# Kernel tuning notes

Measured on AMD Instinct MI355X. Metric: run time of the kernel, lower is better.

The kernel has to match this reference:

```python
import jax, jax.numpy as jnp
import numpy as np

D, H1, O, E = 1024, 4096, 1024, 8
B = 8192


def setup_inputs() -> dict:
    key = jax.random.key(0)
    k1, k2, k3, k4 = jax.random.split(key, 4)
    # kaiming_uniform_ with nonlinearity='relu': bound = sqrt(6 / fan_in), fan_in = last dim
    b_w1 = float(np.sqrt(6.0 / D))
    b_w2 = float(np.sqrt(6.0 / H1))
    x = jax.random.normal(k1, (B, D), dtype=jnp.float32)
    eid = jax.random.randint(k2, (B,), 0, E, dtype=jnp.int32)
    W1 = jax.random.uniform(k3, (E, H1, D), dtype=jnp.float32, minval=-b_w1, maxval=b_w1)
    W2 = jax.random.uniform(k4, (E, O, H1), dtype=jnp.float32, minval=-b_w2, maxval=b_w2)
    b2 = jnp.zeros((E, O), dtype=jnp.float32)
    return {"x": x, "eid": eid, "W1": W1, "W2": W2, "b2": b2}


def reference(x, eid, W1, W2, b2):
    # Per-token expert MLP: y_i = gelu(x_i @ W1[eid_i].T) @ W2[eid_i].T + b2[eid_i]
    # Dense-dispatch formulation: loop over the (small, static) expert axis,
    # compute each expert MLP on all tokens, and select per-token via mask.
    # Math is identical to the sort/gather/scatter original.
    y = jnp.zeros((x.shape[0], W2.shape[1]), dtype=x.dtype)
    for e in range(W1.shape[0]):
        h = jax.nn.gelu(x @ W1[e].T, approximate=False)   # [B, H1]
        y_e = h @ W2[e].T + b2[e]                          # [B, O]
        mask = (eid == e)[:, None].astype(x.dtype)
        y = y + mask * y_e
    return y
```

## Files before the change

kernel.cpp:

```cpp
#include <hip/hip_runtime.h>
#include <hip/hip_bf16.h>
#include <math.h>

constexpr int kD  = 1024;
constexpr int kH1 = 4096;
constexpr int kO  = 1024;
constexpr int kE  = 8;
constexpr int kB  = 8192;

constexpr int BM = 256;
constexpr int MAXT = kB / BM + kE;

typedef __attribute__((ext_vector_type(8))) short short8;
typedef __attribute__((ext_vector_type(4))) float f32x4;

__device__ __forceinline__ unsigned short f2bf(float f) {
  unsigned int u = __float_as_uint(f);
  u += 0x7fffu + ((u >> 16) & 1u);
  return (unsigned short)(u >> 16);
}

__device__ __forceinline__ float gelu_fast(float x) {
  float u = 0.7978845608028654f * (x + 0.044715f * x * x * x);
  float eu = __expf(2.0f * u);
  float th = 1.0f - 2.0f / (eu + 1.0f);
  return 0.5f * x * (1.0f + th);
}

__global__ __launch_bounds__(256) void setup_kernel(const int* __restrict__ eid,
                                                    int* __restrict__ perm,
                                                    int* __restrict__ tiles) {
  __shared__ int cnt[kE];
  __shared__ int off[kE];
  __shared__ int cur[kE];
  int t = threadIdx.x;
  if (t < kE) { cnt[t] = 0; cur[t] = 0; }
  __syncthreads();
  for (int i = t; i < kB; i += 256) atomicAdd(&cnt[eid[i]], 1);
  __syncthreads();
  if (t == 0) {
    int o = 0, nt = 0;
    for (int e = 0; e < kE; ++e) {
      off[e] = o;
      int c = cnt[e];
      for (int r = 0; r < c; r += BM) {
        tiles[nt * 4 + 0] = e;
        tiles[nt * 4 + 1] = o + r;
        tiles[nt * 4 + 2] = (c - r < BM) ? (c - r) : BM;
        tiles[nt * 4 + 3] = 0;
        ++nt;
      }
      o += c;
    }
    for (; nt < MAXT; ++nt) {
      tiles[nt * 4 + 0] = 0; tiles[nt * 4 + 1] = 0;
      tiles[nt * 4 + 2] = 0; tiles[nt * 4 + 3] = 0;
    }
  }
  __syncthreads();
  for (int i = t; i < kB; i += 256) {
    int e = eid[i];
    int p = off[e] + atomicAdd(&cur[e], 1);
    perm[p] = i;
  }
}

__global__ __launch_bounds__(256) void gather_kernel(const float* __restrict__ x,
                                                     const int* __restrict__ perm,
                                                     unsigned short* __restrict__ xg) {
  int idx = blockIdx.x * 256 + threadIdx.x;
  int pos = idx >> 7;
  int c   = (idx & 127) << 3;
  int row = perm[pos];
  const float4* s = (const float4*)(x + (size_t)row * kD + c);
  float4 f0 = s[0], f1 = s[1];
  short8 v;
  v[0] = (short)f2bf(f0.x); v[1] = (short)f2bf(f0.y);
  v[2] = (short)f2bf(f0.z); v[3] = (short)f2bf(f0.w);
  v[4] = (short)f2bf(f1.x); v[5] = (short)f2bf(f1.y);
  v[6] = (short)f2bf(f1.z); v[7] = (short)f2bf(f1.w);
  *(short8*)(xg + (size_t)pos * kD + c) = v;
}

__global__ __launch_bounds__(256) void convert_kernel(const float* __restrict__ src,
                                                      unsigned short* __restrict__ dst,
                                                      int n8) {
  int stride = gridDim.x * 256;
  for (int i = blockIdx.x * 256 + threadIdx.x; i < n8; i += stride) {
    const float4* s = (const float4*)(src + (size_t)i * 8);
    float4 f0 = s[0], f1 = s[1];
    short8 v;
    v[0] = (short)f2bf(f0.x); v[1] = (short)f2bf(f0.y);
    v[2] = (short)f2bf(f0.z); v[3] = (short)f2bf(f0.w);
    v[4] = (short)f2bf(f1.x); v[5] = (short)f2bf(f1.y);
    v[6] = (short)f2bf(f1.z); v[7] = (short)f2bf(f1.w);
    *(short8*)(dst + (size_t)i * 8) = v;
  }
}

template <int K, int N, bool GELU, bool BIAS, bool OUTBF>
__global__ __launch_bounds__(512, 2) void gemm8p_kernel(
    const unsigned short* __restrict__ Amat,
    const unsigned short* __restrict__ Bmat,
    const float* __restrict__ bias,
    const int* __restrict__ tiles,
    const int* __restrict__ perm,
    unsigned short* __restrict__ out_bf,
    float* __restrict__ out_f) {
  extern __shared__ unsigned short lds[];
  constexpr int NKt = K / 64;
  constexpr int Npan = N / 256;

  constexpr int total = MAXT * Npan;
  constexpr int cpx = total >> 3;
  constexpr int nchunks_n = (Npan >= 4) ? (Npan / 4) : 1;
  const int bid = blockIdx.x;
  const int id = (bid & 7) * cpx + (bid >> 3);
  const int chunk = id >> 4;
  const int a16 = id & 15;
  const int ti = (chunk / nchunks_n) * 4 + (a16 & 3);
  const int n0 = ((chunk % nchunks_n) * 4 + (a16 >> 2)) * 256;

  const int e  = tiles[ti * 4 + 0];
  const int rs = tiles[ti * 4 + 1];
  const int nr = tiles[ti * 4 + 2];
  if (nr == 0) return;

  const int t = threadIdx.x;
  const int l = t & 63;
  const int w = t >> 6;
  const int r0 = (w >> 2) * 64;
  const int c0 = (w & 3) * 32;

  const unsigned short* Bp = Bmat + (size_t)e * N * K;

  auto ldsA = [&](int buf, int ha) { return lds + (buf * 2 + ha) * 8192; };
  auto ldsB = [&](int buf, int hb) { return lds + 32768 + (buf * 2 + hb) * 8192; };

  int offA[4][2], offB[2][2];
#pragma unroll
  for (int mr = 0; mr < 4; ++mr)
#pragma unroll
    for (int ks = 0; ks < 2; ++ks) {
      int r = r0 + mr * 16 + (l & 15);
      offA[mr][ks] = r * 64 + ((ks * 32 + (l >> 4) * 8) ^ ((r & 7) << 3));
    }
#pragma unroll
  for (int nc = 0; nc < 2; ++nc)
#pragma unroll
    for (int ks = 0; ks < 2; ++ks) {
      int r = c0 + nc * 16 + (l & 15);
      offB[nc][ks] = r * 64 + ((ks * 32 + (l >> 4) * 8) ^ ((r & 7) << 3));
    }

  auto stage = [&](int H) {
    const int slot = H & 3;
    const int ktS = H >> 2, buf = ktS & 1, k0 = ktS * 64;
#pragma unroll
    for (int i = 0; i < 2; ++i) {
      int elem = (i * 512 + t) * 8;
      int r = elem >> 6, cp = elem & 63;
      int cl = cp ^ ((r & 7) << 3);
      const unsigned short* src;
      unsigned short* dst;
      if (slot == 0 || slot == 3) {
        src = Amat + (size_t)(rs + (slot == 3 ? 128 : 0) + r) * K + k0 + cl;
        dst = ldsA(buf, slot == 3 ? 1 : 0) + elem;
      } else {
        src = Bp + (size_t)(n0 + (slot == 2 ? 128 : 0) + r) * K + k0 + cl;
        dst = ldsB(buf, slot == 2 ? 1 : 0) + elem;
      }
      __builtin_amdgcn_global_load_lds(
          (const __attribute__((address_space(1))) unsigned int*)src,
          (__attribute__((address_space(3))) unsigned int*)dst, 16, 0, 0);
    }
  };

  short8 aF[4][2], bF0[2][2], bF1[2][2];
  f32x4 acc[2][2][4][2] = {};

  auto loadA = [&](int buf, int ha) {
    const unsigned short* base = ldsA(buf, ha);
#pragma unroll
    for (int mr = 0; mr < 4; ++mr)
#pragma unroll
      for (int ks = 0; ks < 2; ++ks)
        aF[mr][ks] = *(const short8*)(base + offA[mr][ks]);
  };
  auto loadB = [&](int buf, int hb, short8 (*bF)[2]) {
    const unsigned short* base = ldsB(buf, hb);
#pragma unroll
    for (int nc = 0; nc < 2; ++nc)
#pragma unroll
      for (int ks = 0; ks < 2; ++ks)
        bF[nc][ks] = *(const short8*)(base + offB[nc][ks]);
  };
  auto mfmaQ = [&](int qr, int qc, short8 (*bF)[2]) {
    __builtin_amdgcn_s_setprio(1);
#pragma unroll
    for (int mr = 0; mr < 4; ++mr)
#pragma unroll
      for (int nc = 0; nc < 2; ++nc)
#pragma unroll
        for (int ks = 0; ks < 2; ++ks)
          acc[qr][qc][mr][nc] = __builtin_amdgcn_mfma_f32_16x16x32_bf16(
              aF[mr][ks], bF[nc][ks], acc[qr][qc][mr][nc], 0, 0, 0);
    __builtin_amdgcn_s_setprio(0);
  };

#pragma unroll
  for (int H = 0; H < 4; ++H) stage(H);
  asm volatile("s_waitcnt vmcnt(4)" ::: "memory");
#pragma unroll
  for (int H = 4; H < 7; ++H) stage(H);

  for (int kt = 0; kt < NKt - 1; ++kt) {
    const int buf = kt & 1;
    asm volatile("s_waitcnt vmcnt(6)" ::: "memory");
    __builtin_amdgcn_s_barrier();
    loadA(buf, 0);
    loadB(buf, 0, bF0);
    { int H = 4 * kt + 7;  if (H < 4 * NKt) stage(H); }
    __builtin_amdgcn_s_barrier();
    mfmaQ(0, 0, bF0);
    __builtin_amdgcn_s_barrier();
    loadB(buf, 1, bF1);
    { int H = 4 * kt + 8;  if (H < 4 * NKt) stage(H); }
    __builtin_amdgcn_s_barrier();
    mfmaQ(0, 1, bF1);
    __builtin_amdgcn_s_barrier();
    loadA(buf, 1);
    { int H = 4 * kt + 9;  if (H < 4 * NKt) stage(H); }
    __builtin_amdgcn_s_barrier();
    mfmaQ(1, 0, bF0);
    __builtin_amdgcn_s_barrier();
    { int H = 4 * kt + 10; if (H < 4 * NKt) stage(H); }
    __builtin_amdgcn_s_barrier();
    mfmaQ(1, 1, bF1);
  }
  {
    const int buf = (NKt - 1) & 1;
    asm volatile("s_waitcnt vmcnt(0)" ::: "memory");
    __builtin_amdgcn_s_barrier();
    loadA(buf, 0);
    loadB(buf, 0, bF0);
    __builtin_amdgcn_s_barrier();
    mfmaQ(0, 0, bF0);
    __builtin_amdgcn_s_barrier();
    loadB(buf, 1, bF1);
    __builtin_amdgcn_s_barrier();
    mfmaQ(0, 1, bF1);
    __builtin_amdgcn_s_barrier();
    loadA(buf, 1);
    __builtin_amdgcn_s_barrier();
    mfmaQ(1, 0, bF0);
    __builtin_amdgcn_s_barrier();
    mfmaQ(1, 1, bF1);
  }

  const int lr4 = (l >> 4) * 4;
  const int lc  = l & 15;
#pragma unroll
  for (int qr = 0; qr < 2; ++qr)
#pragma unroll
    for (int mr = 0; mr < 4; ++mr)
#pragma unroll
      for (int rg = 0; rg < 4; ++rg) {
        int row = qr * 128 + r0 + mr * 16 + lr4 + rg;
        if (row < nr) {
          if constexpr (OUTBF) {
            unsigned short* dst = out_bf + (size_t)(rs + row) * N + n0;
#pragma unroll
            for (int qc = 0; qc < 2; ++qc)
#pragma unroll
              for (int nc = 0; nc < 2; ++nc) {
                float v = acc[qr][qc][mr][nc][rg];
                if constexpr (GELU) v = gelu_fast(v);
                dst[qc * 128 + c0 + nc * 16 + lc] = f2bf(v);
              }
          } else {
            int orig = perm[rs + row];
            float* dst = out_f + (size_t)orig * N + n0;
#pragma unroll
            for (int qc = 0; qc < 2; ++qc)
#pragma unroll
              for (int nc = 0; nc < 2; ++nc) {
                float v = acc[qr][qc][mr][nc][rg];
                if constexpr (BIAS)
                  v += bias[(size_t)e * N + n0 + qc * 128 + c0 + nc * 16 + lc];
                dst[qc * 128 + c0 + nc * 16 + lc] = v;
              }
          }
        }
      }
}

extern "C" void kernel_launch(void* const* d_in, const int* in_sizes, int n_in,
                              void* d_out, int out_size, void* d_ws, size_t ws_size,
                              hipStream_t stream) {
  const float* x  = (const float*)d_in[0];
  const int*  eid = (const int*)d_in[1];
  const float* W1 = (const float*)d_in[2];
  const float* W2 = (const float*)d_in[3];
  const float* b2 = (const float*)d_in[4];
  float* y = (float*)d_out;

  char* ws = (char*)d_ws;
  int* perm  = (int*)ws;
  int* tiles = (int*)(ws + 32768);
  unsigned short* xg = (unsigned short*)(ws + 36864);
  size_t xg_bytes = (size_t)(kB + BM) * kD * 2;
  unsigned short* h  = (unsigned short*)(ws + 36864 + xg_bytes);
  size_t h_bytes = (size_t)(kB + BM) * kH1 * 2;
  unsigned short* Wb = (unsigned short*)(ws + 36864 + xg_bytes + h_bytes);

  constexpr int kWelems8 = kE * kH1 * kD / 8;

  auto g1 = gemm8p_kernel<kD, kH1, true, false, true>;
  auto g2 = gemm8p_kernel<kH1, kO, false, true, false>;
  hipFuncSetAttribute((const void*)g1, hipFuncAttributeMaxDynamicSharedMemorySize, 131072);
  hipFuncSetAttribute((const void*)g2, hipFuncAttributeMaxDynamicSharedMemorySize, 131072);

  setup_kernel<<<1, 256, 0, stream>>>(eid, perm, tiles);
  gather_kernel<<<(kB * kD / 8) / 256, 256, 0, stream>>>(x, perm, xg);

  convert_kernel<<<2048, 256, 0, stream>>>(W1, Wb, kWelems8);
  g1<<<MAXT * (kH1 / 256), 512, 131072, stream>>>(xg, Wb, nullptr, tiles, perm, h, nullptr);

  convert_kernel<<<2048, 256, 0, stream>>>(W2, Wb, kWelems8);
  g2<<<MAXT * (kO / 256), 512, 131072, stream>>>(h, Wb, b2, tiles, perm, nullptr, y);
}
```

Baseline: 321.1 us.

## Use 128-row tiles and split-K for second GEMM with reduction kernel

Shrinks the row tile from 256 to 128 (tiles 128x256 with a 3-slot LDS double buffer), restructures the k-loop into two half-steps with a simpler pipeline, and splits the second GEMM's K dimension in two, one half written to fp32 output and the other to a bf16 scratch buffer (reusing xg). A new reduce kernel adds the bf16 partial and the bias into y. The aim is less padding waste from expert tile boundaries and more blocks to fill the CUs for the small-N second GEMM. The cost is an extra pass over y, lower per-block data reuse, and bf16 rounding of one partial sum.

```diff
diff --git a/kernel.cpp b/kernel.cpp
--- a/kernel.cpp
+++ b/kernel.cpp
@@ -8,7 +8,7 @@
 constexpr int kE  = 8;
 constexpr int kB  = 8192;
 
-constexpr int BM = 256;
+constexpr int BM   = 128;
 constexpr int MAXT = kB / BM + kE;
 
 typedef __attribute__((ext_vector_type(8))) short short8;
@@ -18,6 +18,9 @@
   unsigned int u = __float_as_uint(f);
   u += 0x7fffu + ((u >> 16) & 1u);
   return (unsigned short)(u >> 16);
+}
+__device__ __forceinline__ float bf2f(unsigned short u) {
+  return __uint_as_float(((unsigned int)u) << 16);
 }
 
 __device__ __forceinline__ float gelu_fast(float x) {
@@ -98,28 +101,32 @@
   }
 }
 
-template <int K, int N, bool GELU, bool BIAS, bool OUTBF>
-__global__ __launch_bounds__(512, 2) void gemm8p_kernel(
+template <int KTOT, int KTILES, int N, int NPAN, int MODE>
+__global__ __launch_bounds__(512, 2) void gemm2p_kernel(
     const unsigned short* __restrict__ Amat,
     const unsigned short* __restrict__ Bmat,
-    const float* __restrict__ bias,
     const int* __restrict__ tiles,
     const int* __restrict__ perm,
     unsigned short* __restrict__ out_bf,
     float* __restrict__ out_f) {
   extern __shared__ unsigned short lds[];
-  constexpr int NKt = K / 64;
-  constexpr int Npan = N / 256;
-
-  constexpr int total = MAXT * Npan;
+
+  constexpr int total = MAXT * NPAN;
   constexpr int cpx = total >> 3;
-  constexpr int nchunks_n = (Npan >= 4) ? (Npan / 4) : 1;
+  constexpr int nchN = NPAN / 4;
   const int bid = blockIdx.x;
   const int id = (bid & 7) * cpx + (bid >> 3);
   const int chunk = id >> 4;
   const int a16 = id & 15;
-  const int ti = (chunk / nchunks_n) * 4 + (a16 & 3);
-  const int n0 = ((chunk % nchunks_n) * 4 + (a16 >> 2)) * 256;
+  const int ti = (chunk / nchN) * 4 + (a16 & 3);
+  const int pancol = (chunk % nchN) * 4 + (a16 >> 2);
+
+  int n0, kb, half;
+  if constexpr (MODE == 0) {
+    n0 = pancol * 256; kb = 0; half = 0;
+  } else {
+    half = pancol >> 2; n0 = (pancol & 3) * 256; kb = half * (KTOT / 2);
+  }
 
   const int e  = tiles[ti * 4 + 0];
   const int rs = tiles[ti * 4 + 1];
@@ -130,14 +137,11 @@
   const int l = t & 63;
   const int w = t >> 6;
   const int r0 = (w >> 2) * 64;
-  const int c0 = (w & 3) * 32;
-
-  const unsigned short* Bp = Bmat + (size_t)e * N * K;
-
-  auto ldsA = [&](int buf, int ha) { return lds + (buf * 2 + ha) * 8192; };
-  auto ldsB = [&](int buf, int hb) { return lds + 32768 + (buf * 2 + hb) * 8192; };
-
-  int offA[4][2], offB[2][2];
+  const int wc16 = (w & 3) * 16;
+
+  const unsigned short* Bp = Bmat + (size_t)e * N * KTOT;
+
+  int offA[4][2], offB[4][2];
 #pragma unroll
   for (int mr = 0; mr < 4; ++mr)
 #pragma unroll
@@ -146,153 +150,151 @@
       offA[mr][ks] = r * 64 + ((ks * 32 + (l >> 4) * 8) ^ ((r & 7) << 3));
     }
 #pragma unroll
-  for (int nc = 0; nc < 2; ++nc)
+  for (int j = 0; j < 4; ++j)
 #pragma unroll
     for (int ks = 0; ks < 2; ++ks) {
-      int r = c0 + nc * 16 + (l & 15);
-      offB[nc][ks] = r * 64 + ((ks * 32 + (l >> 4) * 8) ^ ((r & 7) << 3));
-    }
-
-  auto stage = [&](int H) {
-    const int slot = H & 3;
-    const int ktS = H >> 2, buf = ktS & 1, k0 = ktS * 64;
-#pragma unroll
-    for (int i = 0; i < 2; ++i) {
-      int elem = (i * 512 + t) * 8;
-      int r = elem >> 6, cp = elem & 63;
-      int cl = cp ^ ((r & 7) << 3);
-      const unsigned short* src;
-      unsigned short* dst;
-      if (slot == 0 || slot == 3) {
-        src = Amat + (size_t)(rs + (slot == 3 ? 128 : 0) + r) * K + k0 + cl;
-        dst = ldsA(buf, slot == 3 ? 1 : 0) + elem;
-      } else {
-        src = Bp + (size_t)(n0 + (slot == 2 ? 128 : 0) + r) * K + k0 + cl;
-        dst = ldsB(buf, slot == 2 ? 1 : 0) + elem;
-      }
-      __builtin_amdgcn_global_load_lds(
-          (const __attribute__((address_space(1))) unsigned int*)src,
-          (__attribute__((address_space(3))) unsigned int*)dst, 16, 0, 0);
-    }
+      int rB = 64 * (j & 1) + wc16 + (l & 15);
+      offB[j][ks] = (j >> 1) * 8192 + rB * 64 +
+                    ((ks * 32 + (l >> 4) * 8) ^ ((rB & 7) << 3));
+    }
+
+  auto stage = [&](int buf, int k0, int idx) {
+    const int slot = idx >> 1, hf = idx & 1;
+    int elem = (hf * 512 + t) * 8;
+    int r = elem >> 6, cp = elem & 63;
+    int cl = cp ^ ((r & 7) << 3);
+    const unsigned short* src =
+        (slot == 0) ? Amat + (size_t)(rs + r) * KTOT + k0 + cl
+                    : Bp + (size_t)(n0 + (slot - 1) * 128 + r) * KTOT + k0 + cl;
+    unsigned short* dst = lds + buf * 24576 + slot * 8192 + elem;
+    __builtin_amdgcn_global_load_lds(
+        (const __attribute__((address_space(1))) unsigned int*)src,
+        (__attribute__((address_space(3))) unsigned int*)dst, 16, 0, 0);
   };
 
-  short8 aF[4][2], bF0[2][2], bF1[2][2];
-  f32x4 acc[2][2][4][2] = {};
-
-  auto loadA = [&](int buf, int ha) {
-    const unsigned short* base = ldsA(buf, ha);
+  short8 aF[4][2], bF[4][2];
+  f32x4 acc[4][4] = {};
+
+  auto readA = [&](int buf) {
+    const unsigned short* base = lds + buf * 24576;
 #pragma unroll
     for (int mr = 0; mr < 4; ++mr)
 #pragma unroll
       for (int ks = 0; ks < 2; ++ks)
         aF[mr][ks] = *(const short8*)(base + offA[mr][ks]);
   };
-  auto loadB = [&](int buf, int hb, short8 (*bF)[2]) {
-    const unsigned short* base = ldsB(buf, hb);
-#pragma unroll
-    for (int nc = 0; nc < 2; ++nc)
+  auto readB = [&](int buf, int jlo) {
+    const unsigned short* base = lds + buf * 24576 + 8192;
+#pragma unroll
+    for (int j = 0; j < 2; ++j)
 #pragma unroll
       for (int ks = 0; ks < 2; ++ks)
-        bF[nc][ks] = *(const short8*)(base + offB[nc][ks]);
+        bF[jlo + j][ks] = *(const short8*)(base + offB[jlo + j][ks]);
   };
-  auto mfmaQ = [&](int qr, int qc, short8 (*bF)[2]) {
+  auto mfmaH = [&](int jlo) {
     __builtin_amdgcn_s_setprio(1);
 #pragma unroll
-    for (int mr = 0; mr < 4; ++mr)
-#pragma unroll
-      for (int nc = 0; nc < 2; ++nc)
+    for (int j = 0; j < 2; ++j)
+#pragma unroll
+      for (int mr = 0; mr < 4; ++mr)
 #pragma unroll
         for (int ks = 0; ks < 2; ++ks)
-          acc[qr][qc][mr][nc] = __builtin_amdgcn_mfma_f32_16x16x32_bf16(
-              aF[mr][ks], bF[nc][ks], acc[qr][qc][mr][nc], 0, 0, 0);
+          acc[jlo + j][mr] = __builtin_amdgcn_mfma_f32_16x16x32_bf16(
+              aF[mr][ks], bF[jlo + j][ks], acc[jlo + j][mr], 0, 0, 0);
     __builtin_amdgcn_s_setprio(0);
   };
 
 #pragma unroll
-  for (int H = 0; H < 4; ++H) stage(H);
-  asm volatile("s_waitcnt vmcnt(4)" ::: "memory");
-#pragma unroll
-  for (int H = 4; H < 7; ++H) stage(H);
-
-  for (int kt = 0; kt < NKt - 1; ++kt) {
+  for (int idx = 0; idx < 6; ++idx) stage(0, kb, idx);
+
+  for (int kt = 0; kt < KTILES - 1; ++kt) {
     const int buf = kt & 1;
-    asm volatile("s_waitcnt vmcnt(6)" ::: "memory");
-    __builtin_amdgcn_s_barrier();
-    loadA(buf, 0);
-    loadB(buf, 0, bF0);
-    { int H = 4 * kt + 7;  if (H < 4 * NKt) stage(H); }
-    __builtin_amdgcn_s_barrier();
-    mfmaQ(0, 0, bF0);
-    __builtin_amdgcn_s_barrier();
-    loadB(buf, 1, bF1);
-    { int H = 4 * kt + 8;  if (H < 4 * NKt) stage(H); }
-    __builtin_amdgcn_s_barrier();
-    mfmaQ(0, 1, bF1);
-    __builtin_amdgcn_s_barrier();
-    loadA(buf, 1);
-    { int H = 4 * kt + 9;  if (H < 4 * NKt) stage(H); }
-    __builtin_amdgcn_s_barrier();
-    mfmaQ(1, 0, bF0);
-    __builtin_amdgcn_s_barrier();
-    { int H = 4 * kt + 10; if (H < 4 * NKt) stage(H); }
-    __builtin_amdgcn_s_barrier();
-    mfmaQ(1, 1, bF1);
+    const int nb = buf ^ 1;
+    const int k0n = kb + (kt + 1) * 64;
+    asm volatile("s_waitcnt vmcnt(2)" ::: "memory");
+    __builtin_amdgcn_s_barrier();
+    readA(buf);
+    readB(buf, 0);
+    stage(nb, k0n, 0); stage(nb, k0n, 1); stage(nb, k0n, 2);
+    __builtin_amdgcn_s_barrier();
+    mfmaH(0);
+    asm volatile("s_waitcnt vmcnt(3)" ::: "memory");
+    __builtin_amdgcn_s_barrier();
+    readB(buf, 2);
+    stage(nb, k0n, 3); stage(nb, k0n, 4); stage(nb, k0n, 5);
+    __builtin_amdgcn_s_barrier();
+    mfmaH(2);
   }
   {
-    const int buf = (NKt - 1) & 1;
+    const int buf = (KTILES - 1) & 1;
+    asm volatile("s_waitcnt vmcnt(2)" ::: "memory");
+    __builtin_amdgcn_s_barrier();
+    readA(buf);
+    readB(buf, 0);
+    __builtin_amdgcn_s_barrier();
+    mfmaH(0);
     asm volatile("s_waitcnt vmcnt(0)" ::: "memory");
     __builtin_amdgcn_s_barrier();
-    loadA(buf, 0);
-    loadB(buf, 0, bF0);
-    __builtin_amdgcn_s_barrier();
-    mfmaQ(0, 0, bF0);
-    __builtin_amdgcn_s_barrier();
-    loadB(buf, 1, bF1);
-    __builtin_amdgcn_s_barrier();
-    mfmaQ(0, 1, bF1);
-    __builtin_amdgcn_s_barrier();
-    loadA(buf, 1);
-    __builtin_amdgcn_s_barrier();
-    mfmaQ(1, 0, bF0);
-    __builtin_amdgcn_s_barrier();
-    mfmaQ(1, 1, bF1);
+    readB(buf, 2);
+    __builtin_amdgcn_s_barrier();
+    mfmaH(2);
   }
 
   const int lr4 = (l >> 4) * 4;
   const int lc  = l & 15;
 #pragma unroll
-  for (int qr = 0; qr < 2; ++qr)
-#pragma unroll
-    for (int mr = 0; mr < 4; ++mr)
-#pragma unroll
-      for (int rg = 0; rg < 4; ++rg) {
-        int row = qr * 128 + r0 + mr * 16 + lr4 + rg;
-        if (row < nr) {
-          if constexpr (OUTBF) {
+  for (int mr = 0; mr < 4; ++mr)
+#pragma unroll
+    for (int rg = 0; rg < 4; ++rg) {
+      int row = r0 + mr * 16 + lr4 + rg;
+      if (row < nr) {
+        if constexpr (MODE == 0) {
+          unsigned short* dst = out_bf + (size_t)(rs + row) * N + n0;
+#pragma unroll
+          for (int j = 0; j < 4; ++j)
+            dst[j * 64 + wc16 + lc] = f2bf(gelu_fast(acc[j][mr][rg]));
+        } else {
+          if (half == 0) {
+            float* dst = out_f + (size_t)perm[rs + row] * N + n0;
+#pragma unroll
+            for (int j = 0; j < 4; ++j)
+              dst[j * 64 + wc16 + lc] = acc[j][mr][rg];
+          } else {
             unsigned short* dst = out_bf + (size_t)(rs + row) * N + n0;
 #pragma unroll
-            for (int qc = 0; qc < 2; ++qc)
-#pragma unroll
-              for (int nc = 0; nc < 2; ++nc) {
-                float v = acc[qr][qc][mr][nc][rg];
-                if constexpr (GELU) v = gelu_fast(v);
-                dst[qc * 128 + c0 + nc * 16 + lc] = f2bf(v);
-              }
-          } else {
-            int orig = perm[rs + row];
-            float* dst = out_f + (size_t)orig * N + n0;
-#pragma unroll
-            for (int qc = 0; qc < 2; ++qc)
-#pragma unroll
-              for (int nc = 0; nc < 2; ++nc) {
-                float v = acc[qr][qc][mr][nc][rg];
-                if constexpr (BIAS)
-                  v += bias[(size_t)e * N + n0 + qc * 128 + c0 + nc * 16 + lc];
-                dst[qc * 128 + c0 + nc * 16 + lc] = v;
-              }
+            for (int j = 0; j < 4; ++j)
+              dst[j * 64 + wc16 + lc] = f2bf(acc[j][mr][rg]);
           }
         }
       }
+    }
+}
+
+__global__ __launch_bounds__(256) void reduce_kernel(float* __restrict__ y,
+                                                     const unsigned short* __restrict__ part,
+                                                     const int* __restrict__ perm,
+                                                     const int* __restrict__ eid,
+                                                     const float* __restrict__ b2) {
+  int idx = blockIdx.x * 256 + threadIdx.x;
+  int p = idx >> 7;
+  int c = (idx & 127) << 3;
+  int orig = perm[p];
+  int e = eid[orig];
+  float* yp = y + (size_t)orig * kO + c;
+  short8 pv = *(const short8*)(part + (size_t)p * kO + c);
+  const float* bp = b2 + (size_t)e * kO + c;
+  float4 y0 = *(float4*)yp, y1 = *(float4*)(yp + 4);
+  float4 b0 = *(const float4*)bp, b1 = *(const float4*)(bp + 4);
+  y0.x += bf2f((unsigned short)pv[0]) + b0.x;
+  y0.y += bf2f((unsigned short)pv[1]) + b0.y;
+  y0.z += bf2f((unsigned short)pv[2]) + b0.z;
+  y0.w += bf2f((unsigned short)pv[3]) + b0.w;
+  y1.x += bf2f((unsigned short)pv[4]) + b1.x;
+  y1.y += bf2f((unsigned short)pv[5]) + b1.y;
+  y1.z += bf2f((unsigned short)pv[6]) + b1.z;
+  y1.w += bf2f((unsigned short)pv[7]) + b1.w;
+  *(float4*)yp = y0;
+  *(float4*)(yp + 4) = y1;
 }
 
 extern "C" void kernel_launch(void* const* d_in, const int* in_sizes, int n_in,
@@ -309,24 +311,26 @@
   int* perm  = (int*)ws;
   int* tiles = (int*)(ws + 32768);
   unsigned short* xg = (unsigned short*)(ws + 36864);
-  size_t xg_bytes = (size_t)(kB + BM) * kD * 2;
+  size_t xg_bytes = (size_t)(kB + 256) * kD * 2;
   unsigned short* h  = (unsigned short*)(ws + 36864 + xg_bytes);
-  size_t h_bytes = (size_t)(kB + BM) * kH1 * 2;
+  size_t h_bytes = (size_t)(kB + 256) * kH1 * 2;
   unsigned short* Wb = (unsigned short*)(ws + 36864 + xg_bytes + h_bytes);
 
   constexpr int kWelems8 = kE * kH1 * kD / 8;
 
-  auto g1 = gemm8p_kernel<kD, kH1, true, false, true>;
-  auto g2 = gemm8p_kernel<kH1, kO, false, true, false>;
-  hipFuncSetAttribute((const void*)g1, hipFuncAttributeMaxDynamicSharedMemorySize, 131072);
-  hipFuncSetAttribute((const void*)g2, hipFuncAttributeMaxDynamicSharedMemorySize, 131072);
+  auto g1 = gemm2p_kernel<kD, 16, kH1, 16, 0>;
+  auto g2 = gemm2p_kernel<kH1, 32, kO, 8, 1>;
+  hipFuncSetAttribute((const void*)g1, hipFuncAttributeMaxDynamicSharedMemorySize, 98304);
+  hipFuncSetAttribute((const void*)g2, hipFuncAttributeMaxDynamicSharedMemorySize, 98304);
 
   setup_kernel<<<1, 256, 0, stream>>>(eid, perm, tiles);
   gather_kernel<<<(kB * kD / 8) / 256, 256, 0, stream>>>(x, perm, xg);
 
   convert_kernel<<<2048, 256, 0, stream>>>(W1, Wb, kWelems8);
-  g1<<<MAXT * (kH1 / 256), 512, 131072, stream>>>(xg, Wb, nullptr, tiles, perm, h, nullptr);
+  g1<<<MAXT * 16, 512, 98304, stream>>>(xg, Wb, tiles, perm, h, nullptr);
 
   convert_kernel<<<2048, 256, 0, stream>>>(W2, Wb, kWelems8);
-  g2<<<MAXT * (kO / 256), 512, 131072, stream>>>(h, Wb, b2, tiles, perm, nullptr, y);
-}
+  g2<<<MAXT * 8, 512, 98304, stream>>>(h, Wb, tiles, perm, xg, y);
+
+  reduce_kernel<<<(kB * kO / 8) / 256, 256, 0, stream>>>(y, xg, perm, eid, b2);
+}
```

New measurement: 340.4 us. +6.0%, slower.

## Fuse x gather with W1 conversion and fold W2 conversion into GEMM1 tail

Applied to the files above, without the earlier changes.

Merges the token gather/bf16 cast and the W1 fp32-to-bf16 conversion into a single grid-stride kernel, which removes one launch and its tail. When the workspace is large enough for separate W1/W2 bf16 buffers, GEMM1 blocks convert W2 after finishing their tile, and blocks with empty tiles convert straight away instead of exiting. This lets the memory-bound W2 conversion overlap GEMM1 compute and drops another launch. The cost is that GEMM1 blocks get longer and compete for bandwidth, and the code needs a second 64MB workspace buffer, with the old sequential path kept as a fallback.

```diff
diff --git a/kernel.cpp b/kernel.cpp
--- a/kernel.cpp
+++ b/kernel.cpp
@@ -65,21 +65,35 @@
   }
 }
 
-__global__ __launch_bounds__(256) void gather_kernel(const float* __restrict__ x,
-                                                     const int* __restrict__ perm,
-                                                     unsigned short* __restrict__ xg) {
-  int idx = blockIdx.x * 256 + threadIdx.x;
-  int pos = idx >> 7;
-  int c   = (idx & 127) << 3;
-  int row = perm[pos];
-  const float4* s = (const float4*)(x + (size_t)row * kD + c);
-  float4 f0 = s[0], f1 = s[1];
-  short8 v;
-  v[0] = (short)f2bf(f0.x); v[1] = (short)f2bf(f0.y);
-  v[2] = (short)f2bf(f0.z); v[3] = (short)f2bf(f0.w);
-  v[4] = (short)f2bf(f1.x); v[5] = (short)f2bf(f1.y);
-  v[6] = (short)f2bf(f1.z); v[7] = (short)f2bf(f1.w);
-  *(short8*)(xg + (size_t)pos * kD + c) = v;
+constexpr int kGN = kB * kD / 8;
+constexpr int kCN = kE * kH1 * kD / 8;
+
+__global__ __launch_bounds__(256) void gatherconv_kernel(
+    const float* __restrict__ x, const int* __restrict__ perm,
+    unsigned short* __restrict__ xg,
+    const float* __restrict__ W1, unsigned short* __restrict__ W1b) {
+  const int stride = gridDim.x * 256;
+  for (int u = blockIdx.x * 256 + threadIdx.x; u < kGN + kCN; u += stride) {
+    const float4* s;
+    unsigned short* d;
+    if (u < kGN) {
+      int pos = u >> 7;
+      int c   = (u & 127) << 3;
+      s = (const float4*)(x + (size_t)perm[pos] * kD + c);
+      d = xg + (size_t)pos * kD + c;
+    } else {
+      size_t v = (size_t)(u - kGN) * 8;
+      s = (const float4*)(W1 + v);
+      d = W1b + v;
+    }
+    float4 f0 = s[0], f1 = s[1];
+    short8 o;
+    o[0] = (short)f2bf(f0.x); o[1] = (short)f2bf(f0.y);
+    o[2] = (short)f2bf(f0.z); o[3] = (short)f2bf(f0.w);
+    o[4] = (short)f2bf(f1.x); o[5] = (short)f2bf(f1.y);
+    o[6] = (short)f2bf(f1.z); o[7] = (short)f2bf(f1.w);
+    *(short8*)d = o;
+  }
 }
 
 __global__ __launch_bounds__(256) void convert_kernel(const float* __restrict__ src,
@@ -98,7 +112,9 @@
   }
 }
 
-template <int K, int N, bool GELU, bool BIAS, bool OUTBF>
+constexpr int kCN2 = kE * kO * kH1 / 8;
+
+template <int K, int N, bool GELU, bool BIAS, bool OUTBF, bool CONVTAIL>
 __global__ __launch_bounds__(512, 2) void gemm8p_kernel(
     const unsigned short* __restrict__ Amat,
     const unsigned short* __restrict__ Bmat,
@@ -106,7 +122,9 @@
     const int* __restrict__ tiles,
     const int* __restrict__ perm,
     unsigned short* __restrict__ out_bf,
-    float* __restrict__ out_f) {
+    float* __restrict__ out_f,
+    const float* __restrict__ csrc,
+    unsigned short* __restrict__ cdst) {
   extern __shared__ unsigned short lds[];
   constexpr int NKt = K / 64;
   constexpr int Npan = N / 256;
@@ -124,7 +142,6 @@
   const int e  = tiles[ti * 4 + 0];
   const int rs = tiles[ti * 4 + 1];
   const int nr = tiles[ti * 4 + 2];
-  if (nr == 0) return;
 
   const int t = threadIdx.x;
   const int l = t & 63;
@@ -132,167 +149,183 @@
   const int r0 = (w >> 2) * 64;
   const int c0 = (w & 3) * 32;
 
-  const unsigned short* Bp = Bmat + (size_t)e * N * K;
-
-  auto ldsA = [&](int buf, int ha) { return lds + (buf * 2 + ha) * 8192; };
-  auto ldsB = [&](int buf, int hb) { return lds + 32768 + (buf * 2 + hb) * 8192; };
-
-  int offA[4][2], offB[2][2];
-#pragma unroll
-  for (int mr = 0; mr < 4; ++mr)
-#pragma unroll
-    for (int ks = 0; ks < 2; ++ks) {
-      int r = r0 + mr * 16 + (l & 15);
-      offA[mr][ks] = r * 64 + ((ks * 32 + (l >> 4) * 8) ^ ((r & 7) << 3));
-    }
-#pragma unroll
-  for (int nc = 0; nc < 2; ++nc)
-#pragma unroll
-    for (int ks = 0; ks < 2; ++ks) {
-      int r = c0 + nc * 16 + (l & 15);
-      offB[nc][ks] = r * 64 + ((ks * 32 + (l >> 4) * 8) ^ ((r & 7) << 3));
-    }
-
-  auto stage = [&](int H) {
-    const int slot = H & 3;
-    const int ktS = H >> 2, buf = ktS & 1, k0 = ktS * 64;
-#pragma unroll
-    for (int i = 0; i < 2; ++i) {
-      int elem = (i * 512 + t) * 8;
-      int r = elem >> 6, cp = elem & 63;
-      int cl = cp ^ ((r & 7) << 3);
-      const unsigned short* src;
-      unsigned short* dst;
-      if (slot == 0 || slot == 3) {
-        src = Amat + (size_t)(rs + (slot == 3 ? 128 : 0) + r) * K + k0 + cl;
-        dst = ldsA(buf, slot == 3 ? 1 : 0) + elem;
-      } else {
-        src = Bp + (size_t)(n0 + (slot == 2 ? 128 : 0) + r) * K + k0 + cl;
-        dst = ldsB(buf, slot == 2 ? 1 : 0) + elem;
+  if (nr != 0) {
+    const unsigned short* Bp = Bmat + (size_t)e * N * K;
+
+    auto ldsA = [&](int buf, int ha) { return lds + (buf * 2 + ha) * 8192; };
+    auto ldsB = [&](int buf, int hb) { return lds + 32768 + (buf * 2 + hb) * 8192; };
+
+    int offA[4][2], offB[2][2];
+#pragma unroll
+    for (int mr = 0; mr < 4; ++mr)
+#pragma unroll
+      for (int ks = 0; ks < 2; ++ks) {
+        int r = r0 + mr * 16 + (l & 15);
+        offA[mr][ks] = r * 64 + ((ks * 32 + (l >> 4) * 8) ^ ((r & 7) << 3));
       }
-      __builtin_amdgcn_global_load_lds(
-          (const __attribute__((address_space(1))) unsigned int*)src,
-          (__attribute__((address_space(3))) unsigned int*)dst, 16, 0, 0);
-    }
-  };
-
-  short8 aF[4][2], bF0[2][2], bF1[2][2];
-  f32x4 acc[2][2][4][2] = {};
-
-  auto loadA = [&](int buf, int ha) {
-    const unsigned short* base = ldsA(buf, ha);
-#pragma unroll
-    for (int mr = 0; mr < 4; ++mr)
-#pragma unroll
-      for (int ks = 0; ks < 2; ++ks)
-        aF[mr][ks] = *(const short8*)(base + offA[mr][ks]);
-  };
-  auto loadB = [&](int buf, int hb, short8 (*bF)[2]) {
-    const unsigned short* base = ldsB(buf, hb);
 #pragma unroll
     for (int nc = 0; nc < 2; ++nc)
 #pragma unroll
-      for (int ks = 0; ks < 2; ++ks)
-        bF[nc][ks] = *(const short8*)(base + offB[nc][ks]);
-  };
-  auto mfmaQ = [&](int qr, int qc, short8 (*bF)[2]) {
-    __builtin_amdgcn_s_setprio(1);
-#pragma unroll
-    for (int mr = 0; mr < 4; ++mr)
+      for (int ks = 0; ks < 2; ++ks) {
+        int r = c0 + nc * 16 + (l & 15);
+        offB[nc][ks] = r * 64 + ((ks * 32 + (l >> 4) * 8) ^ ((r & 7) << 3));
+      }
+
+    auto stage = [&](int H) {
+      const int slot = H & 3;
+      const int ktS = H >> 2, buf = ktS & 1, k0 = ktS * 64;
+#pragma unroll
+      for (int i = 0; i < 2; ++i) {
+        int elem = (i * 512 + t) * 8;
+        int r = elem >> 6, cp = elem & 63;
+        int cl = cp ^ ((r & 7) << 3);
+        const unsigned short* src;
+        unsigned short* dst;
+        if (slot == 0 || slot == 3) {
+          src = Amat + (size_t)(rs + (slot == 3 ? 128 : 0) + r) * K + k0 + cl;
+          dst = ldsA(buf, slot == 3 ? 1 : 0) + elem;
+        } else {
+          src = Bp + (size_t)(n0 + (slot == 2 ? 128 : 0) + r) * K + k0 + cl;
+          dst = ldsB(buf, slot == 2 ? 1 : 0) + elem;
+        }
+        __builtin_amdgcn_global_load_lds(
+            (const __attribute__((address_space(1))) unsigned int*)src,
+            (__attribute__((address_space(3))) unsigned int*)dst, 16, 0, 0);
+      }
+    };
+
+    short8 aF[4][2], bF0[2][2], bF1[2][2];
+    f32x4 acc[2][2][4][2] = {};
+
+    auto loadA = [&](int buf, int ha) {
+      const unsigned short* base = ldsA(buf, ha);
+#pragma unroll
+      for (int mr = 0; mr < 4; ++mr)
+#pragma unroll
+        for (int ks = 0; ks < 2; ++ks)
+          aF[mr][ks] = *(const short8*)(base + offA[mr][ks]);
+    };
+    auto loadB = [&](int buf, int hb, short8 (*bF)[2]) {
+      const unsigned short* base = ldsB(buf, hb);
 #pragma unroll
       for (int nc = 0; nc < 2; ++nc)
 #pragma unroll
         for (int ks = 0; ks < 2; ++ks)
-          acc[qr][qc][mr][nc] = __builtin_amdgcn_mfma_f32_16x16x32_bf16(
-              aF[mr][ks], bF[nc][ks], acc[qr][qc][mr][nc], 0, 0, 0);
-    __builtin_amdgcn_s_setprio(0);
-  };
-
-#pragma unroll
-  for (int H = 0; H < 4; ++H) stage(H);
-  asm volatile("s_waitcnt vmcnt(4)" ::: "memory");
-#pragma unroll
-  for (int H = 4; H < 7; ++H) stage(H);
-
-  for (int kt = 0; kt < NKt - 1; ++kt) {
-    const int buf = kt & 1;
-    asm volatile("s_waitcnt vmcnt(6)" ::: "memory");
-    __builtin_amdgcn_s_barrier();
-    loadA(buf, 0);
-    loadB(buf, 0, bF0);
-    { int H = 4 * kt + 7;  if (H < 4 * NKt) stage(H); }
-    __builtin_amdgcn_s_barrier();
-    mfmaQ(0, 0, bF0);
-    __builtin_amdgcn_s_barrier();
-    loadB(buf, 1, bF1);
-    { int H = 4 * kt + 8;  if (H < 4 * NKt) stage(H); }
-    __builtin_amdgcn_s_barrier();
-    mfmaQ(0, 1, bF1);
-    __builtin_amdgcn_s_barrier();
-    loadA(buf, 1);
-    { int H = 4 * kt + 9;  if (H < 4 * NKt) stage(H); }
-    __builtin_amdgcn_s_barrier();
-    mfmaQ(1, 0, bF0);
-    __builtin_amdgcn_s_barrier();
-    { int H = 4 * kt + 10; if (H < 4 * NKt) stage(H); }
-    __builtin_amdgcn_s_barrier();
-    mfmaQ(1, 1, bF1);
-  }
-  {
-    const int buf = (NKt - 1) & 1;
-    asm volatile("s_waitcnt vmcnt(0)" ::: "memory");
-    __builtin_amdgcn_s_barrier();
-    loadA(buf, 0);
-    loadB(buf, 0, bF0);
-    __builtin_amdgcn_s_barrier();
-    mfmaQ(0, 0, bF0);
-    __builtin_amdgcn_s_barrier();
-    loadB(buf, 1, bF1);
-    __builtin_amdgcn_s_barrier();
-    mfmaQ(0, 1, bF1);
-    __builtin_amdgcn_s_barrier();
-    loadA(buf, 1);
-    __builtin_amdgcn_s_barrier();
-    mfmaQ(1, 0, bF0);
-    __builtin_amdgcn_s_barrier();
-    mfmaQ(1, 1, bF1);
-  }
-
-  const int lr4 = (l >> 4) * 4;
-  const int lc  = l & 15;
-#pragma unroll
-  for (int qr = 0; qr < 2; ++qr)
-#pragma unroll
-    for (int mr = 0; mr < 4; ++mr)
-#pragma unroll
-      for (int rg = 0; rg < 4; ++rg) {
-        int row = qr * 128 + r0 + mr * 16 + lr4 + rg;
-        if (row < nr) {
-          if constexpr (OUTBF) {
-            unsigned short* dst = out_bf + (size_t)(rs + row) * N + n0;
-#pragma unroll
-            for (int qc = 0; qc < 2; ++qc)
-#pragma unroll
-              for (int nc = 0; nc < 2; ++nc) {
-                float v = acc[qr][qc][mr][nc][rg];
-                if constexpr (GELU) v = gelu_fast(v);
-                dst[qc * 128 + c0 + nc * 16 + lc] = f2bf(v);
-              }
-          } else {
-            int orig = perm[rs + row];
-            float* dst = out_f + (size_t)orig * N + n0;
-#pragma unroll
-            for (int qc = 0; qc < 2; ++qc)
-#pragma unroll
-              for (int nc = 0; nc < 2; ++nc) {
-                float v = acc[qr][qc][mr][nc][rg];
-                if constexpr (BIAS)
-                  v += bias[(size_t)e * N + n0 + qc * 128 + c0 + nc * 16 + lc];
-                dst[qc * 128 + c0 + nc * 16 + lc] = v;
-              }
+          bF[nc][ks] = *(const short8*)(base + offB[nc][ks]);
+    };
+    auto mfmaQ = [&](int qr, int qc, short8 (*bF)[2]) {
+      __builtin_amdgcn_s_setprio(1);
+#pragma unroll
+      for (int mr = 0; mr < 4; ++mr)
+#pragma unroll
+        for (int nc = 0; nc < 2; ++nc)
+#pragma unroll
+          for (int ks = 0; ks < 2; ++ks)
+            acc[qr][qc][mr][nc] = __builtin_amdgcn_mfma_f32_16x16x32_bf16(
+                aF[mr][ks], bF[nc][ks], acc[qr][qc][mr][nc], 0, 0, 0);
+      __builtin_amdgcn_s_setprio(0);
+    };
+
+#pragma unroll
+    for (int H = 0; H < 4; ++H) stage(H);
+    asm volatile("s_waitcnt vmcnt(4)" ::: "memory");
+#pragma unroll
+    for (int H = 4; H < 7; ++H) stage(H);
+
+    for (int kt = 0; kt < NKt - 1; ++kt) {
+      const int buf = kt & 1;
+      asm volatile("s_waitcnt vmcnt(6)" ::: "memory");
+      __builtin_amdgcn_s_barrier();
+      loadA(buf, 0);
+      loadB(buf, 0, bF0);
+      { int H = 4 * kt + 7;  if (H < 4 * NKt) stage(H); }
+      __builtin_amdgcn_s_barrier();
+      mfmaQ(0, 0, bF0);
+      __builtin_amdgcn_s_barrier();
+      loadB(buf, 1, bF1);
+      { int H = 4 * kt + 8;  if (H < 4 * NKt) stage(H); }
+      __builtin_amdgcn_s_barrier();
+      mfmaQ(0, 1, bF1);
+      __builtin_amdgcn_s_barrier();
+      loadA(buf, 1);
+      { int H = 4 * kt + 9;  if (H < 4 * NKt) stage(H); }
+      __builtin_amdgcn_s_barrier();
+      mfmaQ(1, 0, bF0);
+      __builtin_amdgcn_s_barrier();
+      { int H = 4 * kt + 10; if (H < 4 * NKt) stage(H); }
+      __builtin_amdgcn_s_barrier();
+      mfmaQ(1, 1, bF1);
+    }
+    {
+      const int buf = (NKt - 1) & 1;
+      asm volatile("s_waitcnt vmcnt(0)" ::: "memory");
+      __builtin_amdgcn_s_barrier();
+      loadA(buf, 0);
+      loadB(buf, 0, bF0);
+      __builtin_amdgcn_s_barrier();
+      mfmaQ(0, 0, bF0);
+      __builtin_amdgcn_s_barrier();
+      loadB(buf, 1, bF1);
+      __builtin_amdgcn_s_barrier();
+      mfmaQ(0, 1, bF1);
+      __builtin_amdgcn_s_barrier();
+      loadA(buf, 1);
+      __builtin_amdgcn_s_barrier();
+      mfmaQ(1, 0, bF0);
+      __builtin_amdgcn_s_barrier();
+      mfmaQ(1, 1, bF1);
+    }
+
+    const int lr4 = (l >> 4) * 4;
+    const int lc  = l & 15;
+#pragma unroll
+    for (int qr = 0; qr < 2; ++qr)
+#pragma unroll
+      for (int mr = 0; mr < 4; ++mr)
+#pragma unroll
+        for (int rg = 0; rg < 4; ++rg) {
+          int row = qr * 128 + r0 + mr * 16 + lr4 + rg;
+          if (row < nr) {
+            if constexpr (OUTBF) {
+              unsigned short* dst = out_bf + (size_t)(rs + row) * N + n0;
+#pragma unroll
+              for (int qc = 0; qc < 2; ++qc)
+#pragma unroll
+                for (int nc = 0; nc < 2; ++nc) {
+                  float v = acc[qr][qc][mr][nc][rg];
+                  if constexpr (GELU) v = gelu_fast(v);
+                  dst[qc * 128 + c0 + nc * 16 + lc] = f2bf(v);
+                }
+            } else {
+              int orig = perm[rs + row];
+              float* dst = out_f + (size_t)orig * N + n0;
+#pragma unroll
+              for (int qc = 0; qc < 2; ++qc)
+#pragma unroll
+                for (int nc = 0; nc < 2; ++nc) {
+                  float v = acc[qr][qc][mr][nc][rg];
+                  if constexpr (BIAS)
+                    v += bias[(size_t)e * N + n0 + qc * 128 + c0 + nc * 16 + lc];
+                  dst[qc * 128 + c0 + nc * 16 + lc] = v;
+                }
+            }
           }
         }
-      }
+  }
+
+  if constexpr (CONVTAIL) {
+    const size_t stride = (size_t)gridDim.x * 512;
+    for (size_t u = (size_t)bid * 512 + t; u < (size_t)kCN2; u += stride) {
+      const float4* s = (const float4*)(csrc + u * 8);
+      float4 f0 = s[0], f1 = s[1];
+      short8 v;
+      v[0] = (short)f2bf(f0.x); v[1] = (short)f2bf(f0.y);
+      v[2] = (short)f2bf(f0.z); v[3] = (short)f2bf(f0.w);
+      v[4] = (short)f2bf(f1.x); v[5] = (short)f2bf(f1.y);
+      v[6] = (short)f2bf(f1.z); v[7] = (short)f2bf(f1.w);
+      *(short8*)(cdst + u * 8) = v;
+    }
+  }
 }
 
 extern "C" void kernel_launch(void* const* d_in, const int* in_sizes, int n_in,
@@ -309,24 +342,35 @@
   int* perm  = (int*)ws;
   int* tiles = (int*)(ws + 32768);
   unsigned short* xg = (unsigned short*)(ws + 36864);
-  size_t xg_bytes = (size_t)(kB + BM) * kD * 2;
+  size_t xg_bytes = (size_t)(kB + 256) * kD * 2;
   unsigned short* h  = (unsigned short*)(ws + 36864 + xg_bytes);
-  size_t h_bytes = (size_t)(kB + BM) * kH1 * 2;
-  unsigned short* Wb = (unsigned short*)(ws + 36864 + xg_bytes + h_bytes);
-
-  constexpr int kWelems8 = kE * kH1 * kD / 8;
-
-  auto g1 = gemm8p_kernel<kD, kH1, true, false, true>;
-  auto g2 = gemm8p_kernel<kH1, kO, false, true, false>;
-  hipFuncSetAttribute((const void*)g1, hipFuncAttributeMaxDynamicSharedMemorySize, 131072);
-  hipFuncSetAttribute((const void*)g2, hipFuncAttributeMaxDynamicSharedMemorySize, 131072);
+  size_t h_bytes = (size_t)(kB + 256) * kH1 * 2;
+  size_t w1b_off = 36864 + xg_bytes + h_bytes;
+  unsigned short* W1b = (unsigned short*)(ws + w1b_off);
+  size_t w2b_off = w1b_off + 67108864;
+  const bool twobuf = ws_size >= w2b_off + 67108864;
+  unsigned short* W2b = twobuf ? (unsigned short*)(ws + w2b_off) : W1b;
+
+  auto g1f = gemm8p_kernel<kD, kH1, true, false, true, true>;
+  auto g1s = gemm8p_kernel<kD, kH1, true, false, true, false>;
+  auto g2  = gemm8p_kernel<kH1, kO, false, true, false, false>;
+  hipFuncSetAttribute((const void*)g1f, hipFuncAttributeMaxDynamicSharedMemorySize, 131072);
+  hipFuncSetAttribute((const void*)g1s, hipFuncAttributeMaxDynamicSharedMemorySize, 131072);
+  hipFuncSetAttribute((const void*)g2,  hipFuncAttributeMaxDynamicSharedMemorySize, 131072);
 
   setup_kernel<<<1, 256, 0, stream>>>(eid, perm, tiles);
-  gather_kernel<<<(kB * kD / 8) / 256, 256, 0, stream>>>(x, perm, xg);
-
-  convert_kernel<<<2048, 256, 0, stream>>>(W1, Wb, kWelems8);
-  g1<<<MAXT * (kH1 / 256), 512, 131072, stream>>>(xg, Wb, nullptr, tiles, perm, h, nullptr);
-
-  convert_kernel<<<2048, 256, 0, stream>>>(W2, Wb, kWelems8);
-  g2<<<MAXT * (kO / 256), 512, 131072, stream>>>(h, Wb, b2, tiles, perm, nullptr, y);
-}
+
+  gatherconv_kernel<<<2048, 256, 0, stream>>>(x, perm, xg, W1, W1b);
+
+  if (twobuf) {
+    g1f<<<MAXT * (kH1 / 256), 512, 131072, stream>>>(
+        xg, W1b, nullptr, tiles, perm, h, nullptr, W2, W2b);
+  } else {
+    g1s<<<MAXT * (kH1 / 256), 512, 131072, stream>>>(
+        xg, W1b, nullptr, tiles, perm, h, nullptr, nullptr, nullptr);
+    convert_kernel<<<2048, 256, 0, stream>>>(W2, W2b, kCN2);
+  }
+
+  g2<<<MAXT * (kO / 256), 512, 131072, stream>>>(
+      h, W2b, b2, tiles, perm, nullptr, y, nullptr, nullptr);
+}
```

New measurement: 319.5 us. About the same (-0.5%).
